# Kernel optimization log

Measured on AMD Instinct MI355X. Metric: run time of the kernel, lower is better.

The kernel has to match this reference:

```python
import jax, jax.numpy as jnp
import numpy as np
from jax import lax

B, L, D_MODEL = 4, 1024, 512
D_STATE, D_CONV, D_INNER = 16, 4, 2 * D_MODEL


def setup_inputs() -> dict:
    key = jax.random.key(0)
    ks = jax.random.split(key, 8)
    s = 0.02
    x = jax.random.normal(ks[0], (B, L, D_MODEL), dtype=jnp.float32)
    W_in = jax.random.normal(ks[1], (D_MODEL, 2 * D_INNER), dtype=jnp.float32) * s
    conv_w = jax.random.normal(ks[2], (D_INNER, 1, D_CONV), dtype=jnp.float32) * s  # OIH, depthwise
    conv_b = jnp.zeros((D_INNER,), jnp.float32)
    W_x = jax.random.normal(ks[3], (D_INNER, 2 * D_STATE), dtype=jnp.float32) * s
    W_dt = jax.random.normal(ks[4], (D_INNER, D_INNER), dtype=jnp.float32) * s
    b_dt = jnp.zeros((D_INNER,), jnp.float32)
    # A_log = -logspace(log10(0.001), log10(1.0), d_state); used directly as A in the scan
    A_log = -jnp.logspace(np.log10(1e-3), 0.0, D_STATE, dtype=jnp.float32)
    D_skip = jnp.ones((D_INNER,), jnp.float32) * 0.1
    W_out = jax.random.normal(ks[5], (D_INNER, D_MODEL), dtype=jnp.float32) * s
    gamma = jnp.ones((D_MODEL,), jnp.float32)
    beta = jnp.zeros((D_MODEL,), jnp.float32)
    return dict(x=x, W_in=W_in, conv_w=conv_w, conv_b=conv_b, W_x=W_x, W_dt=W_dt,
                b_dt=b_dt, A_log=A_log, D_skip=D_skip, W_out=W_out, gamma=gamma, beta=beta)


def _mamba_forward(x, W_in, conv_w, conv_b, W_x, W_dt, b_dt, A_log, D_skip, W_out, gamma, beta):
    x = jnp.clip(x, -10.0, 10.0)
    x_and_res = x @ W_in                                  # [B, L, 2*d_inner]
    xp, res = jnp.split(x_and_res, 2, axis=-1)
    # Depthwise causal conv1d: torch pads d_conv-1 both sides then slices [:L] -> left-pad only.
    xt = jnp.transpose(xp, (0, 2, 1))                     # [B, d_inner, L]
    xc = lax.conv_general_dilated(xt, conv_w, window_strides=(1,),
                                  padding=[(D_CONV - 1, 0)],
                                  dimension_numbers=('NCH', 'OIH', 'NCH'),
                                  feature_group_count=D_INNER)
    xc = xc + conv_b[None, :, None]
    xc = jax.nn.silu(jnp.transpose(xc, (0, 2, 1)))        # [B, L, d_inner]
    ssm = xc @ W_x                                        # [B, L, 2*d_state]
    Bm, Cm = jnp.split(ssm, 2, axis=-1)                   # each [B, L, d_state]
    delta = xc @ W_dt + b_dt                              # [B, L, d_inner] (no softplus in source)

    # Selective scan over time (sequential recurrence)
    def step(h, inp):
        u_t, d_t, B_t, C_t = inp                          # [B,I], [B,I], [B,S], [B,S]
        dA = jnp.exp(jnp.clip(d_t[:, :, None] * A_log, -5.0, 5.0))   # [B, I, S]
        h = dA * h + (d_t[:, :, None] * B_t[:, None, :]) * u_t[:, :, None]
        y = jnp.einsum('bis,bs->bi', h, C_t)
        return h, y

    tm = lambda a: jnp.swapaxes(a, 0, 1)                  # time-major
    h0 = jnp.zeros((x.shape[0], D_INNER, D_STATE), xc.dtype)
    _, ys = lax.scan(step, h0, (tm(xc), tm(delta), tm(Bm), tm(Cm)))
    y = jnp.swapaxes(ys, 0, 1) + xc * D_skip              # D skip connection

    y = y * jax.nn.silu(res)                              # gating
    out = y @ W_out
    r = out + x                                           # residual
    mu = jnp.mean(r, axis=-1, keepdims=True)
    var = jnp.var(r, axis=-1, keepdims=True)
    return gamma * (r - mu) / jnp.sqrt(var + 1e-5) + beta


def reference(x, W_in, conv_w, conv_b, W_x, W_dt, b_dt, A_log, D_skip, W_out, gamma, beta):
    return _mamba_forward(x, W_in, conv_w, conv_b, W_x, W_dt, b_dt, A_log, D_skip, W_out, gamma, beta)
```

## Files before the change

### kernel.cpp

```cpp
#include <hip/hip_runtime.h>
#include <hip/hip_bf16.h>

typedef __hip_bfloat16 bf16;
typedef unsigned short ushort_t;
typedef unsigned int uint_t;
typedef __attribute__((ext_vector_type(8))) __bf16 bf16x8;
typedef __attribute__((ext_vector_type(8))) ushort_t u16x8;
typedef __attribute__((ext_vector_type(4))) ushort_t u16x4;
typedef __attribute__((ext_vector_type(4))) float f32x4;
typedef __attribute__((ext_vector_type(2))) float f32x2;

#define BB 4
#define LL 1024
#define DM 512
#define DS 16
#define DI 1024
#define ROWS 4096
#define NC 64
#define CT 16
#define NDTX 1152
#define LOG2E 1.4426950408889634f

__device__ __forceinline__ float b2f(bf16 v) { return __bfloat162float(v); }

__device__ __forceinline__ float load_flag(const void* src, int i, int isbf)
{
    return isbf ? b2f(((const bf16*)src)[i]) : ((const float*)src)[i];
}

__device__ __forceinline__ ushort_t f2b_bits(float v)
{
    bf16 t = __float2bfloat16(v);
    return *(ushort_t*)&t;
}

__device__ __forceinline__ float bits2f(ushort_t u)
{
    uint_t w = ((uint_t)u) << 16;
    return __uint_as_float(w);
}

__device__ __forceinline__ float exp2fast(float x)
{
#if __has_builtin(__builtin_amdgcn_exp2f)
    return __builtin_amdgcn_exp2f(x);
#else
    float r;
    asm("v_exp_f32 %0, %1" : "=v"(r) : "v"(x));
    return r;
#endif
}

__device__ __forceinline__ int detect_local(const ushort_t* wdt)
{
    __shared__ int bad;
    if (threadIdx.x == 0) bad = 0;
    __syncthreads();
    ushort_t u = wdt[threadIdx.x & 255];
    if (((u >> 7) & 0xFF) >= 127) atomicAdd(&bad, 1);
    __syncthreads();
    return (bad <= 8) ? 1 : 0;
}

__global__ __launch_bounds__(256)
void prep_all(const void* x, const void* Win, const void* Wdt, const void* Wx,
              const void* Wout, const void* cw, const void* cb, const void* Alog,
              const void* Dsk, const void* gam, const void* bet, const void* bdtin,
              bf16* __restrict__ xbf, bf16* __restrict__ WtIn,
              bf16* __restrict__ WtDtx, bf16* __restrict__ WtOut,
              float* __restrict__ ccw, float* __restrict__ ccb,
              float* __restrict__ cAlg, float* __restrict__ cDsk,
              float* __restrict__ cgam, float* __restrict__ cbet,
              float* __restrict__ bdtx)
{
    const int isbf = detect_local((const ushort_t*)Wdt);
    int blk = blockIdx.x;

    if (blk < 2048) {
        int idx = blk * 256 + threadIdx.x;
        float v[4];
        if (isbf) {
            uint2 raw = ((const uint2*)x)[idx];
            v[0] = __uint_as_float(raw.x << 16);
            v[1] = __uint_as_float(raw.x & 0xFFFF0000u);
            v[2] = __uint_as_float(raw.y << 16);
            v[3] = __uint_as_float(raw.y & 0xFFFF0000u);
        } else {
            float4 raw = ((const float4*)x)[idx];
            v[0] = raw.x; v[1] = raw.y; v[2] = raw.z; v[3] = raw.w;
        }
        uint_t b0, b1;
        b0 = f2b_bits(fminf(fmaxf(v[0], -10.f), 10.f))
           | ((uint_t)f2b_bits(fminf(fmaxf(v[1], -10.f), 10.f)) << 16);
        b1 = f2b_bits(fminf(fmaxf(v[2], -10.f), 10.f))
           | ((uint_t)f2b_bits(fminf(fmaxf(v[3], -10.f), 10.f)) << 16);
        uint2 ow; ow.x = b0; ow.y = b1;
        ((uint2*)xbf)[idx] = ow;
    } else if (blk < 4640) {
        int tb = blk - 2048;
        const void* src; bf16* dst; int K, Nsrc, tpr;
        if (tb < 1024)      { src = Win;  dst = WtIn;   K = 512;  Nsrc = 2048; tpr = 64; }
        else if (tb < 2048) { tb -= 1024; src = Wdt;  dst = WtDtx; K = 1024; Nsrc = 1024; tpr = 32; }
        else if (tb < 2080) { tb -= 2048; src = Wx;   dst = WtDtx + 1024 * 1024; K = 1024; Nsrc = 32; tpr = 1; }
        else                { tb -= 2080; src = Wout; dst = WtOut;  K = 1024; Nsrc = 512;  tpr = 16; }
        int k0 = (tb / tpr) * 32, n0 = (tb % tpr) * 32;

        __shared__ float tile[32][33];
        int tx = threadIdx.x & 31, ty = threadIdx.x >> 5;
        #pragma unroll
        for (int j = 0; j < 4; ++j)
            tile[ty + 8 * j][tx] = load_flag(src, (k0 + ty + 8 * j) * Nsrc + n0 + tx, isbf);
        __syncthreads();
        #pragma unroll
        for (int j = 0; j < 4; ++j)
            dst[(size_t)(n0 + ty + 8 * j) * K + k0 + tx] = __float2bfloat16(tile[tx][ty + 8 * j]);
    } else {
        int i = (blk - 4640) * 256 + threadIdx.x;
        if (i < 4096)        ccw[i] = load_flag(cw, i, isbf);
        else if (i < 5120)   ccb[i - 4096] = load_flag(cb, i - 4096, isbf);
        else if (i < 5136)   cAlg[i - 5120] = load_flag(Alog, i - 5120, isbf) * LOG2E;
        else if (i < 6160)   cDsk[i - 5136] = load_flag(Dsk, i - 5136, isbf);
        else if (i < 6672)   cgam[i - 6160] = load_flag(gam, i - 6160, isbf);
        else if (i < 7184)   cbet[i - 6672] = load_flag(bet, i - 6672, isbf);
        else if (i < 8336) {
            int j = i - 7184;
            bdtx[j] = (j < DI) ? load_flag(bdtin, j, isbf) : 0.f;
        } else if (i < 106640) {
            (WtDtx + 1056 * 1024)[i - 8336] = __float2bfloat16(0.f);
        }
    }
}

__device__ __forceinline__ void gload16(const bf16* g, ushort_t* l)
{
    __builtin_amdgcn_global_load_lds(
        (const __attribute__((address_space(1))) void*)g,
        (__attribute__((address_space(3))) void*)l, 16, 0, 0);
}

template <int TM, int TN, bool OBF, bool OT, bool SPLIT>
__global__ __launch_bounds__(256)
void gemm_mfma(const bf16* __restrict__ A, const bf16* __restrict__ Bt,
               const float* __restrict__ bias, void* __restrict__ Cv,
               void* __restrict__ Cv2, int M, int N, int K)
{
    constexpr int MI = TM / 32, NJ = TN / 32;
    constexpr int NQA = TM * 8 / 256;
    constexpr int NQB = TN * 8 / 256;
    __shared__ ushort_t As[TM * 64];
    __shared__ ushort_t Bs[TN * 64];

    const int tid = threadIdx.x;
    const int lane = tid & 63;
    const int w = tid >> 6;
    const int wr = w >> 1, wc = w & 1;

    const int nbx = gridDim.x;
    const int nwg = nbx * gridDim.y;
    int flat = blockIdx.y * nbx + blockIdx.x;
    if ((nwg & 7) == 0) {
        const int cpx = nwg >> 3;
        flat = (flat & 7) * cpx + (flat >> 3);
    }
    const int m0 = (flat / nbx) * TM;
    const int n0 = (flat % nbx) * TN;

    const bf16* gA[NQA]; ushort_t* lA[NQA];
    #pragma unroll
    for (int q = 0; q < NQA; ++q) {
        int p = q * 256 + tid;
        int row = p >> 3, kc = ((p & 7) - row) & 7;
        gA[q] = A + (size_t)(m0 + row) * K + kc * 8;
        lA[q] = &As[(q * 256 + w * 64) * 8];
    }
    const bf16* gB[NQB]; ushort_t* lB[NQB];
    #pragma unroll
    for (int q = 0; q < NQB; ++q) {
        int p = q * 256 + tid;
        int row = p >> 3, kc = ((p & 7) - row) & 7;
        gB[q] = Bt + (size_t)(n0 + row) * K + kc * 8;
        lB[q] = &Bs[(q * 256 + w * 64) * 8];
    }

    f32x4 acc[MI][NJ];
    #pragma unroll
    for (int i = 0; i < MI; ++i)
        #pragma unroll
        for (int j = 0; j < NJ; ++j)
            acc[i][j] = (f32x4){0.f, 0.f, 0.f, 0.f};

    const int ko = lane >> 4;
    const int ml = lane & 15;

    for (int k0 = 0; k0 < K; k0 += 64) {
        #pragma unroll
        for (int q = 0; q < NQA; ++q) gload16(gA[q] + k0, lA[q]);
        #pragma unroll
        for (int q = 0; q < NQB; ++q) gload16(gB[q] + k0, lB[q]);
        __syncthreads();

        #pragma unroll
        for (int half = 0; half < 2; ++half) {
            bf16x8 af[MI], bfr[NJ];
            #pragma unroll
            for (int i = 0; i < MI; ++i) {
                int m = wr * (TM / 2) + i * 16 + ml;
                af[i] = *(const bf16x8*)&As[(m * 8 + ((half * 4 + ko + m) & 7)) * 8];
            }
            #pragma unroll
            for (int j = 0; j < NJ; ++j) {
                int n = wc * (TN / 2) + j * 16 + ml;
                bfr[j] = *(const bf16x8*)&Bs[(n * 8 + ((half * 4 + ko + n) & 7)) * 8];
            }
            #pragma unroll
            for (int i = 0; i < MI; ++i)
                #pragma unroll
                for (int j = 0; j < NJ; ++j)
                    acc[i][j] = __builtin_amdgcn_mfma_f32_16x16x32_bf16(
                        af[i], bfr[j], acc[i][j], 0, 0, 0);
        }
        __syncthreads();
    }

    const int rq = lane >> 4;
    #pragma unroll
    for (int j = 0; j < NJ; ++j) {
        int n = n0 + wc * (TN / 2) + j * 16 + ml;
        float bv = bias ? bias[n] : 0.f;
        #pragma unroll
        for (int i = 0; i < MI; ++i) {
            int mb = m0 + wr * (TM / 2) + i * 16 + rq * 4;
            if (SPLIT && n >= 1024) {
                if (n < 1088) {
                    #pragma unroll
                    for (int r = 0; r < 4; ++r)
                        ((float*)Cv2)[(size_t)(mb + r) * 64 + (n - 1024)] =
                            acc[i][j][r] + bv;
                }
            } else if (OT) {
                u16x4 pk;
                #pragma unroll
                for (int r = 0; r < 4; ++r)
                    pk[r] = f2b_bits(acc[i][j][r] + bv);
                *(u16x4*)((ushort_t*)Cv + (size_t)n * M + mb) = pk;
            } else {
                #pragma unroll
                for (int r = 0; r < 4; ++r) {
                    float v = acc[i][j][r] + bv;
                    if (OBF) ((bf16*)Cv)[(size_t)(mb + r) * N + n] = __float2bfloat16(v);
                    else     ((float*)Cv)[(size_t)(mb + r) * N + n] = v;
                }
            }
        }
    }
}

__global__ __launch_bounds__(256)
void conv_silu(const bf16* __restrict__ xrbT, const float* __restrict__ cw,
               const float* __restrict__ cb, bf16* __restrict__ xcT,
               bf16* __restrict__ xc)
{
    __shared__ ushort_t tile[64 * 72];
    const int blk = blockIdx.x;
    const int ch0 = (blk & 15) * 64;
    const int T0b = (blk >> 4) * 64;
    const int lc = threadIdx.x >> 2, tg = threadIdx.x & 3;
    const int i = ch0 + lc;
    const int T0 = T0b + tg * 16;

    const ushort_t* base = (const ushort_t*)xrbT + (size_t)i * ROWS + T0;
    u16x8 m0 = *(const u16x8*)base;
    u16x8 m1 = *(const u16x8*)(base + 8);
    u16x8 pv = {0, 0, 0, 0, 0, 0, 0, 0};
    if ((T0 & (LL - 1)) != 0) pv = *(const u16x8*)(base - 8);

    float4 w = ((const float4*)cw)[i];
    float bs = cb[i];
    float xm3 = bits2f(pv[5]), xm2 = bits2f(pv[6]), xm1 = bits2f(pv[7]);
    u16x8 o0, o1;
    #pragma unroll
    for (int tt = 0; tt < 16; ++tt) {
        float x0 = bits2f(tt < 8 ? m0[tt] : m1[tt - 8]);
        float acc = bs;
        acc = fmaf(xm3, w.x, acc);
        acc = fmaf(xm2, w.y, acc);
        acc = fmaf(xm1, w.z, acc);
        acc = fmaf(x0,  w.w, acc);
        ushort_t ob = f2b_bits(acc / (1.f + __expf(-acc)));
        if (tt < 8) o0[tt] = ob; else o1[tt - 8] = ob;
        xm3 = xm2; xm2 = xm1; xm1 = x0;
    }
    ushort_t* dt = (ushort_t*)xcT + (size_t)i * ROWS + T0;
    *(u16x8*)dt = o0;
    *(u16x8*)(dt + 8) = o1;
    *(u16x8*)&tile[lc * 72 + tg * 16] = o0;
    *(u16x8*)&tile[lc * 72 + tg * 16 + 8] = o1;
    __syncthreads();
    const int lt = threadIdx.x >> 2, cg = threadIdx.x & 3;
    u16x8 q0, q1;
    #pragma unroll
    for (int j = 0; j < 8; ++j) q0[j] = tile[(cg * 16 + j) * 72 + lt];
    #pragma unroll
    for (int j = 8; j < 16; ++j) q1[j - 8] = tile[(cg * 16 + j) * 72 + lt];
    ushort_t* wp = (ushort_t*)xc + (size_t)(T0b + lt) * DI + ch0 + cg * 16;
    *(u16x8*)wp = q0;
    *(u16x8*)(wp + 8) = q1;
}

__global__ __launch_bounds__(1024, 4)
void scan_fused(const bf16* __restrict__ xcT, const bf16* __restrict__ dT,
                const float* __restrict__ ssmf, const bf16* __restrict__ xrbT,
                const float* __restrict__ A_l2e, const float* __restrict__ Dskip,
                bf16* __restrict__ ybf)
{
    __shared__ uint_t lsum[DS * 1024];

    const int tid = threadIdx.x;
    const int b = blockIdx.x >> 6;
    const int ch0 = (blockIdx.x & 63) << 4;
    const int chl = tid & 15;
    const int c = tid >> 4;
    const int i = ch0 + chl;
    const size_t tb = (size_t)b * LL + c * CT;

    float a[DS];
    #pragma unroll
    for (int s = 0; s < DS; ++s) {
        uint_t bits = (uint_t)__builtin_amdgcn_readfirstlane((int)__float_as_uint(A_l2e[s]));
        a[s] = __uint_as_float(bits);
    }

    const u16x8* dp = (const u16x8*)((const ushort_t*)dT + (size_t)i * ROWS + tb);
    const u16x8* up = (const u16x8*)((const ushort_t*)xcT + (size_t)i * ROWS + tb);
    const u16x8* rp = (const u16x8*)((const ushort_t*)xrbT + (size_t)(1024 + i) * ROWS + tb);
    const float* sbase = ssmf + tb * 64;

    f32x2 h2[8];
    #pragma unroll
    for (int k = 0; k < 8; ++k) h2[k] = (f32x2){0.f, 0.f};
    float cd = 0.f;

    {
        u16x8 dvlo = dp[0], dvhi = dp[1];
        u16x8 uvlo = up[0], uvhi = up[1];
        f32x4 rB[4], mB[4];
        #pragma unroll
        for (int j = 0; j < 4; ++j) rB[j] = *(const f32x4*)(sbase + j * 4);
        #pragma unroll
        for (int j = 0; j < 4; ++j) mB[j] = *(const f32x4*)(sbase + 64 + j * 4);
        #pragma unroll
        for (int tt = 0; tt < 16; ++tt) {
            f32x4 B[4];
            #pragma unroll
            for (int j = 0; j < 4; ++j) { B[j] = rB[j]; rB[j] = mB[j]; }
            if (tt < 14) {
                #pragma unroll
                for (int j = 0; j < 4; ++j)
                    mB[j] = *(const f32x4*)(sbase + (tt + 2) * 64 + j * 4);
            }
            float dv = bits2f(tt < 8 ? dvlo[tt] : dvhi[tt - 8]);
            float uv = bits2f(tt < 8 ? uvlo[tt] : uvhi[tt - 8]);
            float du = dv * uv;
            cd += dv;
            f32x2 du2 = {du, du};
            f32x2 dv2 = {dv, dv};
            #pragma unroll
            for (int k = 0; k < 8; ++k) {
                f32x2 av = {a[2 * k], a[2 * k + 1]};
                f32x2 e2 = dv2 * av;
                f32x2 dA = {exp2fast(e2[0]), exp2fast(e2[1])};
                f32x2 Bv = {B[k >> 1][(k & 1) * 2], B[k >> 1][(k & 1) * 2 + 1]};
                h2[k] = dA * h2[k] + du2 * Bv;
            }
        }
    }

    f32x2 cdf = {cd, cd};
    #pragma unroll
    for (int k = 0; k < 8; ++k) {
        int s0 = 2 * k, s1 = 2 * k + 1;
        f32x2 av = {a[s0], a[s1]};
        f32x2 e2 = cdf * av;
        f32x2 pc = {exp2fast(e2[0]), exp2fast(e2[1])};
        lsum[s0 * 1024 + (tid ^ ((s0 & 1) << 4))] =
            (uint_t)f2b_bits(pc[0]) | ((uint_t)f2b_bits(h2[k][0]) << 16);
        lsum[s1 * 1024 + (tid ^ ((s1 & 1) << 4))] =
            (uint_t)f2b_bits(pc[1]) | ((uint_t)f2b_bits(h2[k][1]) << 16);
    }
    __syncthreads();

    if (tid < 256) {
        int cl = tid & 15, s = tid >> 4;
        int sx = (s & 1) << 4;
        float hh = 0.f;
        #pragma unroll
        for (int cb = 0; cb < 4; ++cb) {
            uint_t wv[16];
            #pragma unroll
            for (int j = 0; j < 16; ++j)
                wv[j] = lsum[s * 1024 + ((((cb * 16 + j) * 16) + cl) ^ sx)];
            uint_t hs[16];
            #pragma unroll
            for (int j = 0; j < 16; ++j) {
                hs[j] = (uint_t)f2b_bits(hh);
                float pp = bits2f((ushort_t)(wv[j] & 0xFFFF));
                float qq = bits2f((ushort_t)(wv[j] >> 16));
                hh = fmaf(pp, hh, qq);
            }
            #pragma unroll
            for (int j = 0; j < 16; ++j)
                lsum[s * 1024 + ((((cb * 16 + j) * 16) + cl) ^ sx)] = hs[j];
        }
    }
    __syncthreads();

    #pragma unroll
    for (int k = 0; k < 8; ++k) {
        int s0 = 2 * k, s1 = 2 * k + 1;
        h2[k][0] = bits2f((ushort_t)lsum[s0 * 1024 + (tid ^ ((s0 & 1) << 4))]);
        h2[k][1] = bits2f((ushort_t)lsum[s1 * 1024 + (tid ^ ((s1 & 1) << 4))]);
    }

    const float dsk = Dskip[i];

    {
        u16x8 dvlo = dp[0], dvhi = dp[1];
        u16x8 uvlo = up[0], uvhi = up[1];
        u16x8 rvlo = rp[0], rvhi = rp[1];
        f32x4 rB[4], nB[4];
        #pragma unroll
        for (int j = 0; j < 4; ++j) rB[j] = *(const f32x4*)(sbase + j * 4);
        #pragma unroll
        for (int tt = 0; tt < 16; ++tt) {
            f32x4 C[4];
            #pragma unroll
            for (int j = 0; j < 4; ++j)
                C[j] = *(const f32x4*)(sbase + tt * 64 + 16 + j * 4);
            if (tt < 15) {
                #pragma unroll
                for (int j = 0; j < 4; ++j)
                    nB[j] = *(const f32x4*)(sbase + (tt + 1) * 64 + j * 4);
            }
            float dv = bits2f(tt < 8 ? dvlo[tt] : dvhi[tt - 8]);
            float uv = bits2f(tt < 8 ? uvlo[tt] : uvhi[tt - 8]);
            float rs = bits2f(tt < 8 ? rvlo[tt] : rvhi[tt - 8]);
            float du = dv * uv;
            f32x2 du2 = {du, du};
            f32x2 dv2 = {dv, dv};
            #pragma unroll
            for (int k = 0; k < 8; ++k) {
                f32x2 av = {a[2 * k], a[2 * k + 1]};
                f32x2 e2 = dv2 * av;
                f32x2 dA = {exp2fast(e2[0]), exp2fast(e2[1])};
                f32x2 Bv = {rB[k >> 1][(k & 1) * 2], rB[k >> 1][(k & 1) * 2 + 1]};
                h2[k] = dA * h2[k] + du2 * Bv;
            }
            f32x2 y2a = {0.f, 0.f}, y2b = {0.f, 0.f};
            #pragma unroll
            for (int k = 0; k < 8; k += 2) {
                f32x2 Cva = {C[k >> 1][0], C[k >> 1][1]};
                f32x2 Cvb = {C[k >> 1][2], C[k >> 1][3]};
                y2a = y2a + h2[k] * Cva;
                y2b = y2b + h2[k + 1] * Cvb;
            }
            f32x2 y2 = y2a + y2b;
            float y = y2[0] + y2[1];
            float g = rs / (1.f + __expf(-rs));
            ybf[(tb + tt) * DI + i] = __float2bfloat16((y + uv * dsk) * g);
            #pragma unroll
            for (int j = 0; j < 4; ++j) rB[j] = nB[j];
        }
    }
}

__global__ __launch_bounds__(256)
void ln_kernel(const bf16* __restrict__ outp, const void* __restrict__ xsrc,
               const void* __restrict__ wdt_probe,
               const float* __restrict__ gamma, const float* __restrict__ beta,
               void* __restrict__ out)
{
    const int isbf = detect_local((const ushort_t*)wdt_probe);
    const int row = blockIdx.x;
    const int tid = threadIdx.x;

    float r[2];
    float sum = 0.f, ss = 0.f;
    #pragma unroll
    for (int q = 0; q < 2; ++q) {
        int j = tid + q * 256;
        float xv = load_flag(xsrc, row * DM + j, isbf);
        xv = fminf(fmaxf(xv, -10.f), 10.f);
        float v = b2f(outp[(size_t)row * DM + j]) + xv;
        r[q] = v;
        sum += v;
        ss = fmaf(v, v, ss);
    }
    #pragma unroll
    for (int off = 32; off >= 1; off >>= 1) {
        sum += __shfl_down(sum, off);
        ss  += __shfl_down(ss, off);
    }
    __shared__ float s1[4], s2[4];
    __shared__ float stats[2];
    int wid = tid >> 6, lane = tid & 63;
    if (lane == 0) { s1[wid] = sum; s2[wid] = ss; }
    __syncthreads();
    if (tid == 0) {
        float S = s1[0] + s1[1] + s1[2] + s1[3];
        float Qq = s2[0] + s2[1] + s2[2] + s2[3];
        float mean = S / DM;
        float var = Qq / DM - mean * mean;
        stats[0] = mean;
        stats[1] = rsqrtf(var + 1e-5f);
    }
    __syncthreads();
    float mean = stats[0], rstd = stats[1];
    #pragma unroll
    for (int q = 0; q < 2; ++q) {
        int j = tid + q * 256;
        float v = (r[q] - mean) * rstd * gamma[j] + beta[j];
        size_t o = (size_t)row * DM + j;
        if (isbf) ((bf16*)out)[o] = __float2bfloat16(v);
        else      ((float*)out)[o] = v;
    }
}

extern "C" void kernel_launch(void* const* d_in, const int* in_sizes, int n_in,
                              void* d_out, int out_size, void* d_ws, size_t ws_size,
                              hipStream_t stream)
{
    float* W = (float*)d_ws;
    float* ccw  = W;
    float* ccb  = ccw  + 4096;
    float* cAlg = ccb  + 1024;
    float* cDsk = cAlg + 16;
    float* cgam = cDsk + 1024;
    float* cbet = cgam + 512;
    float* bdtx = cbet + 512;
    bf16*  xbf  = (bf16*)(bdtx + 1152);
    bf16*  xrbT = xbf  + 2097152;
    bf16*  xcT  = xrbT + 8388608;
    bf16*  xc   = xcT  + 4194304;
    bf16*  ybf  = xc   + 4194304;
    bf16*  dT   = ybf  + 4194304;
    bf16*  ssm0 = dT   + 4194304;
    bf16*  outp = ssm0 + 262144;
    bf16*  WtIn = outp + 2097152;
    bf16*  WtDtx= WtIn + 1048576;
    bf16*  WtOut= WtDtx+ 1179648;
    float* ssmf = (float*)(WtOut + 524288);

    prep_all<<<5057, 256, 0, stream>>>(
        d_in[0], d_in[1], d_in[5], d_in[4], d_in[9], d_in[2], d_in[3],
        d_in[7], d_in[8], d_in[10], d_in[11], d_in[6],
        xbf, WtIn, WtDtx, WtOut, ccw, ccb, cAlg, cDsk, cgam, cbet, bdtx);

    gemm_mfma<128, 128, true, true, false><<<dim3(2048 / 128, ROWS / 128), 256, 0, stream>>>(
        xbf, WtIn, nullptr, xrbT, nullptr, ROWS, 2048, 512);

    conv_silu<<<1024, 256, 0, stream>>>(xrbT, ccw, ccb, xcT, xc);

    gemm_mfma<64, 128, true, true, true><<<dim3(NDTX / 128, ROWS / 64), 256, 0, stream>>>(
        xc, WtDtx, bdtx, dT, ssmf, ROWS, NDTX, DI);

    scan_fused<<<256, 1024, 0, stream>>>(xcT, dT, ssmf, xrbT, cAlg, cDsk, ybf);

    gemm_mfma<64, 64, true, false, false><<<dim3(DM / 64, ROWS / 64), 256, 0, stream>>>(
        ybf, WtOut, nullptr, outp, nullptr, ROWS, DM, DI);

    ln_kernel<<<ROWS, 256, 0, stream>>>(outp, d_in[0], d_in[5], cgam, cbet, d_out);
}
```

Measured before the change: 190.6 us.

## Compute local chunk outputs in first scan pass, apply carry-in via decay

The chunked selective scan now accumulates the chunk-local output (zero initial state, plus the D-skip term) during the first pass and stores it in a new 64KB shared buffer. The second pass no longer reruns the state recurrence. It adds the contribution of the carried-in state, scaled by exp2 of the cumulative delta times A, contracted with C, then applies the gate. This removes the B loads and the recurrent FMA chain from the second pass. In exchange, shared memory per block doubles, which caps occupancy, and the fixup uses a different floating-point evaluation order.

```diff
diff --git a/kernel.cpp b/kernel.cpp
--- a/kernel.cpp
+++ b/kernel.cpp
@@ -314,6 +314,7 @@
                 bf16* __restrict__ ybf)
 {
     __shared__ uint_t lsum[DS * 1024];
+    __shared__ float ylc[CT * 1024];
 
     const int tid = threadIdx.x;
     const int b = blockIdx.x >> 6;
@@ -335,6 +336,8 @@
     const u16x8* rp = (const u16x8*)((const ushort_t*)xrbT + (size_t)(1024 + i) * ROWS + tb);
     const float* sbase = ssmf + tb * 64;
 
+    const float dsk = Dskip[i];
+
     f32x2 h2[8];
     #pragma unroll
     for (int k = 0; k < 8; ++k) h2[k] = (f32x2){0.f, 0.f};
@@ -343,20 +346,19 @@
     {
         u16x8 dvlo = dp[0], dvhi = dp[1];
         u16x8 uvlo = up[0], uvhi = up[1];
-        f32x4 rB[4], mB[4];
+        f32x4 rB[4], nB[4];
         #pragma unroll
         for (int j = 0; j < 4; ++j) rB[j] = *(const f32x4*)(sbase + j * 4);
         #pragma unroll
-        for (int j = 0; j < 4; ++j) mB[j] = *(const f32x4*)(sbase + 64 + j * 4);
-        #pragma unroll
         for (int tt = 0; tt < 16; ++tt) {
-            f32x4 B[4];
-            #pragma unroll
-            for (int j = 0; j < 4; ++j) { B[j] = rB[j]; rB[j] = mB[j]; }
-            if (tt < 14) {
+            f32x4 C[4];
+            #pragma unroll
+            for (int j = 0; j < 4; ++j)
+                C[j] = *(const f32x4*)(sbase + tt * 64 + 16 + j * 4);
+            if (tt < 15) {
                 #pragma unroll
                 for (int j = 0; j < 4; ++j)
-                    mB[j] = *(const f32x4*)(sbase + (tt + 2) * 64 + j * 4);
+                    nB[j] = *(const f32x4*)(sbase + (tt + 1) * 64 + j * 4);
             }
             float dv = bits2f(tt < 8 ? dvlo[tt] : dvhi[tt - 8]);
             float uv = bits2f(tt < 8 ? uvlo[tt] : uvhi[tt - 8]);
@@ -369,9 +371,21 @@
                 f32x2 av = {a[2 * k], a[2 * k + 1]};
                 f32x2 e2 = dv2 * av;
                 f32x2 dA = {exp2fast(e2[0]), exp2fast(e2[1])};
-                f32x2 Bv = {B[k >> 1][(k & 1) * 2], B[k >> 1][(k & 1) * 2 + 1]};
+                f32x2 Bv = {rB[k >> 1][(k & 1) * 2], rB[k >> 1][(k & 1) * 2 + 1]};
                 h2[k] = dA * h2[k] + du2 * Bv;
             }
+            f32x2 y2a = {0.f, 0.f}, y2b = {0.f, 0.f};
+            #pragma unroll
+            for (int k = 0; k < 8; k += 2) {
+                f32x2 Cva = {C[k >> 1][0], C[k >> 1][1]};
+                f32x2 Cvb = {C[k >> 1][2], C[k >> 1][3]};
+                y2a = y2a + h2[k] * Cva;
+                y2b = y2b + h2[k + 1] * Cvb;
+            }
+            f32x2 y2 = y2a + y2b;
+            ylc[tt * 1024 + tid] = y2[0] + y2[1] + uv * dsk;
+            #pragma unroll
+            for (int j = 0; j < 4; ++j) rB[j] = nB[j];
         }
     }
 
@@ -421,54 +435,38 @@
         h2[k][1] = bits2f((ushort_t)lsum[s1 * 1024 + (tid ^ ((s1 & 1) << 4))]);
     }
 
-    const float dsk = Dskip[i];
-
     {
         u16x8 dvlo = dp[0], dvhi = dp[1];
-        u16x8 uvlo = up[0], uvhi = up[1];
         u16x8 rvlo = rp[0], rvhi = rp[1];
-        f32x4 rB[4], nB[4];
-        #pragma unroll
-        for (int j = 0; j < 4; ++j) rB[j] = *(const f32x4*)(sbase + j * 4);
+        float cd2 = 0.f;
         #pragma unroll
         for (int tt = 0; tt < 16; ++tt) {
             f32x4 C[4];
             #pragma unroll
             for (int j = 0; j < 4; ++j)
                 C[j] = *(const f32x4*)(sbase + tt * 64 + 16 + j * 4);
-            if (tt < 15) {
-                #pragma unroll
-                for (int j = 0; j < 4; ++j)
-                    nB[j] = *(const f32x4*)(sbase + (tt + 1) * 64 + j * 4);
-            }
             float dv = bits2f(tt < 8 ? dvlo[tt] : dvhi[tt - 8]);
-            float uv = bits2f(tt < 8 ? uvlo[tt] : uvhi[tt - 8]);
             float rs = bits2f(tt < 8 ? rvlo[tt] : rvhi[tt - 8]);
-            float du = dv * uv;
-            f32x2 du2 = {du, du};
-            f32x2 dv2 = {dv, dv};
-            #pragma unroll
-            for (int k = 0; k < 8; ++k) {
-                f32x2 av = {a[2 * k], a[2 * k + 1]};
-                f32x2 e2 = dv2 * av;
-                f32x2 dA = {exp2fast(e2[0]), exp2fast(e2[1])};
-                f32x2 Bv = {rB[k >> 1][(k & 1) * 2], rB[k >> 1][(k & 1) * 2 + 1]};
-                h2[k] = dA * h2[k] + du2 * Bv;
-            }
+            cd2 += dv;
+            f32x2 cdv = {cd2, cd2};
             f32x2 y2a = {0.f, 0.f}, y2b = {0.f, 0.f};
             #pragma unroll
             for (int k = 0; k < 8; k += 2) {
+                f32x2 av0 = {a[2 * k], a[2 * k + 1]};
+                f32x2 av1 = {a[2 * k + 2], a[2 * k + 3]};
+                f32x2 e0 = cdv * av0;
+                f32x2 e1 = cdv * av1;
+                f32x2 p0 = {exp2fast(e0[0]), exp2fast(e0[1])};
+                f32x2 p1 = {exp2fast(e1[0]), exp2fast(e1[1])};
                 f32x2 Cva = {C[k >> 1][0], C[k >> 1][1]};
                 f32x2 Cvb = {C[k >> 1][2], C[k >> 1][3]};
-                y2a = y2a + h2[k] * Cva;
-                y2b = y2b + h2[k + 1] * Cvb;
+                y2a = y2a + (p0 * h2[k]) * Cva;
+                y2b = y2b + (p1 * h2[k + 1]) * Cvb;
             }
             f32x2 y2 = y2a + y2b;
-            float y = y2[0] + y2[1];
+            float y = ylc[tt * 1024 + tid] + y2[0] + y2[1];
             float g = rs / (1.f + __expf(-rs));
-            ybf[(tb + tt) * DI + i] = __float2bfloat16((y + uv * dsk) * g);
-            #pragma unroll
-            for (int j = 0; j < 4; ++j) rB[j] = nB[j];
+            ybf[(tb + tt) * DI + i] = __float2bfloat16(y * g);
         }
     }
 }
```

After: 191.9 us. About the same (+0.7%).

## Split selective scan across two blocks per sequence with inter-block carry handoff

Applied to the files above, without the earlier changes.

The scan kernel now launches twice as many blocks, each covering half the sequence with chunks of 8 steps instead of 16. The first-half block publishes its final state to global memory and sets a flag. The second-half block spins on that flag and folds the carried state in using a cumulative decay product now stored next to each local prefix. This doubles parallelism and occupancy for the scan, at the cost of a cross-block dependency. That dependency could deadlock if the producer block is not resident, and it adds flag and state traffic.

```diff
diff --git a/kernel.cpp b/kernel.cpp
--- a/kernel.cpp
+++ b/kernel.cpp
@@ -17,7 +17,7 @@
 #define DI 1024
 #define ROWS 4096
 #define NC 64
-#define CT 16
+#define CT 8
 #define NDTX 1152
 #define LOG2E 1.4426950408889634f
 
@@ -71,7 +71,7 @@
               float* __restrict__ ccw, float* __restrict__ ccb,
               float* __restrict__ cAlg, float* __restrict__ cDsk,
               float* __restrict__ cgam, float* __restrict__ cbet,
-              float* __restrict__ bdtx)
+              float* __restrict__ bdtx, uint_t* __restrict__ flg)
 {
     const int isbf = detect_local((const ushort_t*)Wdt);
     int blk = blockIdx.x;
@@ -127,6 +127,8 @@
             bdtx[j] = (j < DI) ? load_flag(bdtin, j, isbf) : 0.f;
         } else if (i < 106640) {
             (WtDtx + 1056 * 1024)[i - 8336] = __float2bfloat16(0.f);
+        } else if (i < 106896) {
+            flg[i - 106640] = 0u;
         }
     }
 }
@@ -307,21 +309,25 @@
     *(u16x8*)(wp + 8) = q1;
 }
 
-__global__ __launch_bounds__(1024, 4)
+__global__ __launch_bounds__(1024, 8)
 void scan_fused(const bf16* __restrict__ xcT, const bf16* __restrict__ dT,
                 const float* __restrict__ ssmf, const bf16* __restrict__ xrbT,
                 const float* __restrict__ A_l2e, const float* __restrict__ Dskip,
-                bf16* __restrict__ ybf)
+                bf16* __restrict__ ybf, float* __restrict__ gh,
+                uint_t* __restrict__ flg)
 {
     __shared__ uint_t lsum[DS * 1024];
+    __shared__ float h0b[256];
 
     const int tid = threadIdx.x;
-    const int b = blockIdx.x >> 6;
-    const int ch0 = (blockIdx.x & 63) << 4;
+    const int half = blockIdx.x >> 8;
+    const int pr = blockIdx.x & 255;
+    const int b = pr >> 6;
+    const int ch0 = (pr & 63) << 4;
     const int chl = tid & 15;
     const int c = tid >> 4;
     const int i = ch0 + chl;
-    const size_t tb = (size_t)b * LL + c * CT;
+    const size_t tb = (size_t)b * LL + half * 512 + c * CT;
 
     float a[DS];
     #pragma unroll
@@ -341,25 +347,17 @@
     float cd = 0.f;
 
     {
-        u16x8 dvlo = dp[0], dvhi = dp[1];
-        u16x8 uvlo = up[0], uvhi = up[1];
-        f32x4 rB[4], mB[4];
-        #pragma unroll
-        for (int j = 0; j < 4; ++j) rB[j] = *(const f32x4*)(sbase + j * 4);
-        #pragma unroll
-        for (int j = 0; j < 4; ++j) mB[j] = *(const f32x4*)(sbase + 64 + j * 4);
-        #pragma unroll
-        for (int tt = 0; tt < 16; ++tt) {
-            f32x4 B[4];
-            #pragma unroll
-            for (int j = 0; j < 4; ++j) { B[j] = rB[j]; rB[j] = mB[j]; }
-            if (tt < 14) {
-                #pragma unroll
-                for (int j = 0; j < 4; ++j)
-                    mB[j] = *(const f32x4*)(sbase + (tt + 2) * 64 + j * 4);
-            }
-            float dv = bits2f(tt < 8 ? dvlo[tt] : dvhi[tt - 8]);
-            float uv = bits2f(tt < 8 ? uvlo[tt] : uvhi[tt - 8]);
+        u16x8 dv8 = dp[0];
+        u16x8 uv8 = up[0];
+        #pragma unroll
+        for (int tt = 0; tt < CT; ++tt) {
+            const float* srow = sbase + tt * 64;
+            f32x4 B0 = *(const f32x4*)(srow);
+            f32x4 B1 = *(const f32x4*)(srow + 4);
+            f32x4 B2 = *(const f32x4*)(srow + 8);
+            f32x4 B3 = *(const f32x4*)(srow + 12);
+            float dv = bits2f(dv8[tt]);
+            float uv = bits2f(uv8[tt]);
             float du = dv * uv;
             cd += dv;
             f32x2 du2 = {du, du};
@@ -369,7 +367,8 @@
                 f32x2 av = {a[2 * k], a[2 * k + 1]};
                 f32x2 e2 = dv2 * av;
                 f32x2 dA = {exp2fast(e2[0]), exp2fast(e2[1])};
-                f32x2 Bv = {B[k >> 1][(k & 1) * 2], B[k >> 1][(k & 1) * 2 + 1]};
+                f32x4 Bq = (k >> 1) == 0 ? B0 : (k >> 1) == 1 ? B1 : (k >> 1) == 2 ? B2 : B3;
+                f32x2 Bv = {Bq[(k & 1) * 2], Bq[(k & 1) * 2 + 1]};
                 h2[k] = dA * h2[k] + du2 * Bv;
             }
         }
@@ -392,7 +391,7 @@
     if (tid < 256) {
         int cl = tid & 15, s = tid >> 4;
         int sx = (s & 1) << 4;
-        float hh = 0.f;
+        float hh = 0.f, rr = 1.f;
         #pragma unroll
         for (int cb = 0; cb < 4; ++cb) {
             uint_t wv[16];
@@ -402,73 +401,86 @@
             uint_t hs[16];
             #pragma unroll
             for (int j = 0; j < 16; ++j) {
-                hs[j] = (uint_t)f2b_bits(hh);
+                hs[j] = (uint_t)f2b_bits(rr) | ((uint_t)f2b_bits(hh) << 16);
                 float pp = bits2f((ushort_t)(wv[j] & 0xFFFF));
                 float qq = bits2f((ushort_t)(wv[j] >> 16));
                 hh = fmaf(pp, hh, qq);
+                rr *= pp;
             }
             #pragma unroll
             for (int j = 0; j < 16; ++j)
                 lsum[s * 1024 + ((((cb * 16 + j) * 16) + cl) ^ sx)] = hs[j];
         }
+        if (half == 0) atomicExch(&gh[pr * 256 + tid], hh);
+    }
+    __syncthreads();
+
+    if (half == 0) {
+        if (tid == 0) { __threadfence(); atomicExch(&flg[pr], 1u); }
+        if (tid < 256) h0b[tid] = 0.f;
+    } else {
+        if (tid == 0) {
+            while (atomicAdd(&flg[pr], 0u) == 0u) __builtin_amdgcn_s_sleep(2);
+        }
+        __syncthreads();
+        if (tid < 256) h0b[tid] = atomicAdd(&gh[pr * 256 + tid], 0.f);
     }
     __syncthreads();
 
     #pragma unroll
     for (int k = 0; k < 8; ++k) {
         int s0 = 2 * k, s1 = 2 * k + 1;
-        h2[k][0] = bits2f((ushort_t)lsum[s0 * 1024 + (tid ^ ((s0 & 1) << 4))]);
-        h2[k][1] = bits2f((ushort_t)lsum[s1 * 1024 + (tid ^ ((s1 & 1) << 4))]);
+        uint_t w0 = lsum[s0 * 1024 + (tid ^ ((s0 & 1) << 4))];
+        uint_t w1 = lsum[s1 * 1024 + (tid ^ ((s1 & 1) << 4))];
+        float Pp0 = bits2f((ushort_t)(w0 & 0xFFFF));
+        float Pp1 = bits2f((ushort_t)(w1 & 0xFFFF));
+        float hl0 = bits2f((ushort_t)(w0 >> 16));
+        float hl1 = bits2f((ushort_t)(w1 >> 16));
+        h2[k][0] = fmaf(Pp0, h0b[s0 * 16 + chl], hl0);
+        h2[k][1] = fmaf(Pp1, h0b[s1 * 16 + chl], hl1);
     }
 
     const float dsk = Dskip[i];
 
     {
-        u16x8 dvlo = dp[0], dvhi = dp[1];
-        u16x8 uvlo = up[0], uvhi = up[1];
-        u16x8 rvlo = rp[0], rvhi = rp[1];
-        f32x4 rB[4], nB[4];
-        #pragma unroll
-        for (int j = 0; j < 4; ++j) rB[j] = *(const f32x4*)(sbase + j * 4);
-        #pragma unroll
-        for (int tt = 0; tt < 16; ++tt) {
-            f32x4 C[4];
-            #pragma unroll
-            for (int j = 0; j < 4; ++j)
-                C[j] = *(const f32x4*)(sbase + tt * 64 + 16 + j * 4);
-            if (tt < 15) {
-                #pragma unroll
-                for (int j = 0; j < 4; ++j)
-                    nB[j] = *(const f32x4*)(sbase + (tt + 1) * 64 + j * 4);
-            }
-            float dv = bits2f(tt < 8 ? dvlo[tt] : dvhi[tt - 8]);
-            float uv = bits2f(tt < 8 ? uvlo[tt] : uvhi[tt - 8]);
-            float rs = bits2f(tt < 8 ? rvlo[tt] : rvhi[tt - 8]);
+        u16x8 dv8 = dp[0];
+        u16x8 uv8 = up[0];
+        u16x8 rv8 = rp[0];
+        #pragma unroll
+        for (int tt = 0; tt < CT; ++tt) {
+            const float* srow = sbase + tt * 64;
+            f32x4 B0 = *(const f32x4*)(srow);
+            f32x4 B1 = *(const f32x4*)(srow + 4);
+            f32x4 B2 = *(const f32x4*)(srow + 8);
+            f32x4 B3 = *(const f32x4*)(srow + 12);
+            f32x4 C0 = *(const f32x4*)(srow + 16);
+            f32x4 C1 = *(const f32x4*)(srow + 20);
+            f32x4 C2 = *(const f32x4*)(srow + 24);
+            f32x4 C3 = *(const f32x4*)(srow + 28);
+            float dv = bits2f(dv8[tt]);
+            float uv = bits2f(uv8[tt]);
+            float rs = bits2f(rv8[tt]);
             float du = dv * uv;
             f32x2 du2 = {du, du};
             f32x2 dv2 = {dv, dv};
+            f32x2 y2a = {0.f, 0.f}, y2b = {0.f, 0.f};
             #pragma unroll
             for (int k = 0; k < 8; ++k) {
                 f32x2 av = {a[2 * k], a[2 * k + 1]};
                 f32x2 e2 = dv2 * av;
                 f32x2 dA = {exp2fast(e2[0]), exp2fast(e2[1])};
-                f32x2 Bv = {rB[k >> 1][(k & 1) * 2], rB[k >> 1][(k & 1) * 2 + 1]};
+                f32x4 Bq = (k >> 1) == 0 ? B0 : (k >> 1) == 1 ? B1 : (k >> 1) == 2 ? B2 : B3;
+                f32x4 Cq = (k >> 1) == 0 ? C0 : (k >> 1) == 1 ? C1 : (k >> 1) == 2 ? C2 : C3;
+                f32x2 Bv = {Bq[(k & 1) * 2], Bq[(k & 1) * 2 + 1]};
+                f32x2 Cv = {Cq[(k & 1) * 2], Cq[(k & 1) * 2 + 1]};
                 h2[k] = dA * h2[k] + du2 * Bv;
-            }
-            f32x2 y2a = {0.f, 0.f}, y2b = {0.f, 0.f};
-            #pragma unroll
-            for (int k = 0; k < 8; k += 2) {
-                f32x2 Cva = {C[k >> 1][0], C[k >> 1][1]};
-                f32x2 Cvb = {C[k >> 1][2], C[k >> 1][3]};
-                y2a = y2a + h2[k] * Cva;
-                y2b = y2b + h2[k + 1] * Cvb;
+                if (k & 1) y2b = y2b + h2[k] * Cv;
+                else       y2a = y2a + h2[k] * Cv;
             }
             f32x2 y2 = y2a + y2b;
             float y = y2[0] + y2[1];
             float g = rs / (1.f + __expf(-rs));
             ybf[(tb + tt) * DI + i] = __float2bfloat16((y + uv * dsk) * g);
-            #pragma unroll
-            for (int j = 0; j < 4; ++j) rB[j] = nB[j];
         }
     }
 }
@@ -549,11 +561,13 @@
     bf16*  WtDtx= WtIn + 1048576;
     bf16*  WtOut= WtDtx+ 1179648;
     float* ssmf = (float*)(WtOut + 524288);
-
-    prep_all<<<5057, 256, 0, stream>>>(
+    float* gh   = ssmf + 262144;
+    uint_t* flg = (uint_t*)(gh + 65536);
+
+    prep_all<<<5058, 256, 0, stream>>>(
         d_in[0], d_in[1], d_in[5], d_in[4], d_in[9], d_in[2], d_in[3],
         d_in[7], d_in[8], d_in[10], d_in[11], d_in[6],
-        xbf, WtIn, WtDtx, WtOut, ccw, ccb, cAlg, cDsk, cgam, cbet, bdtx);
+        xbf, WtIn, WtDtx, WtOut, ccw, ccb, cAlg, cDsk, cgam, cbet, bdtx, flg);
 
     gemm_mfma<128, 128, true, true, false><<<dim3(2048 / 128, ROWS / 128), 256, 0, stream>>>(
         xbf, WtIn, nullptr, xrbT, nullptr, ROWS, 2048, 512);
@@ -563,7 +577,7 @@
     gemm_mfma<64, 128, true, true, true><<<dim3(NDTX / 128, ROWS / 64), 256, 0, stream>>>(
         xc, WtDtx, bdtx, dT, ssmf, ROWS, NDTX, DI);
 
-    scan_fused<<<256, 1024, 0, stream>>>(xcT, dT, ssmf, xrbT, cAlg, cDsk, ybf);
+    scan_fused<<<512, 1024, 0, stream>>>(xcT, dT, ssmf, xrbT, cAlg, cDsk, ybf, gh, flg);
 
     gemm_mfma<64, 64, true, false, false><<<dim3(DM / 64, ROWS / 64), 256, 0, stream>>>(
         ybf, WtOut, nullptr, outp, nullptr, ROWS, DM, DI);
```

Measured after the change: 197.5 us. 1.04x slower.
